# Performance work log

Hardware: AMD Instinct MI355X
Metric: run time of the kernel (lower is better)

## Reference

```python
import jax, jax.numpy as jnp
import numpy as np

MARGIN = 5.0  # margin_between_clusters


def setup_inputs() -> dict:
    key = jax.random.key(0)
    k1, k2, k3 = jax.random.split(key, 3)
    N, D, K = 262144, 128, 64
    embeddings = jax.random.normal(k1, (N, D), dtype=jnp.float32)
    cluster_labels = jax.random.randint(k2, (N,), 0, K, dtype=jnp.int64)
    centroids = jax.random.normal(k3, (K, D), dtype=jnp.float32)
    return {"embeddings": embeddings, "cluster_labels": cluster_labels, "centroids": centroids}


def reference(embeddings, cluster_labels, centroids):
    # Assumes all K clusters are present in cluster_labels (true w.h.p. for N >> K),
    # matching number_cluster = len(unique(labels)) in the original.
    N, d = embeddings.shape
    K = centroids.shape[0]
    labels = cluster_labels.astype(jnp.int32)

    x2 = jnp.sum(embeddings * embeddings, axis=1, keepdims=True)        # [N,1]
    c2 = jnp.sum(centroids * centroids, axis=1)[None, :]                # [1,K]
    d2 = jnp.maximum(x2 + c2 - 2.0 * (embeddings @ centroids.T), 0.0)  # [N,K]
    dist = jnp.sqrt(d2)

    rows = jnp.arange(N)
    own_d = dist[rows, labels]                 # distance to own centroid
    counts = jax.ops.segment_sum(jnp.ones((N,), embeddings.dtype), labels, num_segments=K)
    safe_counts = jnp.maximum(counts, 1.0)

    # attraction: per cluster, mean of squared distance to own centroid
    attr_per_cluster = jax.ops.segment_sum(own_d * own_d, labels, num_segments=K) / safe_counts
    attraction_loss = jnp.sum(jnp.where(counts > 0, attr_per_cluster, 0.0))

    # repulsion: per cluster, mean over (points_in_cluster x other_centroids) of relu((m - d)^2)
    rep = jax.nn.relu((MARGIN - dist) ** 2)    # [N,K]
    row_other = (jnp.sum(rep, axis=1) - rep[rows, labels]) / (K - 1)
    rep_per_cluster = jax.ops.segment_sum(row_other, labels, num_segments=K) / safe_counts
    repulsion_loss = jnp.sum(jnp.where(counts > 0, rep_per_cluster, 0.0))

    return (attraction_loss + repulsion_loss) / K
```

## Files before the change

kernel.cpp:

```cpp
#include <hip/hip_runtime.h>


constexpr int N = 262144;
constexpr int D = 128;
constexpr int K = 64;

constexpr int GRID = 512;
constexpr int NWAVES = 4;
constexpr int TPW = (N / 32) / (GRID * NWAVES);
constexpr int PANEL = 34 * 32;

typedef __bf16 bf16x4 __attribute__((ext_vector_type(4)));
typedef __bf16 bf16x8 __attribute__((ext_vector_type(8)));
typedef float  f32x16 __attribute__((ext_vector_type(16)));

__global__ __launch_bounds__(256) void dcl_main(
    const float* __restrict__ emb,
    const int*   __restrict__ labels,
    const float* __restrict__ cent,
    float* __restrict__ g_attr,
    float* __restrict__ g_rep,
    int*   __restrict__ g_cnt)
{
    __shared__ bf16x8 sA[2 * 8 * 64];
    __shared__ __align__(16) bf16x4 sPanel[NWAVES * PANEL];
    __shared__ float  s_c2[K];
    __shared__ float  s_attr[K];
    __shared__ float  s_rep[K];
    __shared__ int    s_cnt[K];

    const int tid  = threadIdx.x;
    const int wave = tid >> 6;
    const int lane = tid & 63;
    const int l31  = lane & 31;
    const int h    = lane >> 5;

    const int tile0 = (blockIdx.x * NWAVES + wave) * TPW;

    float4 buf[16];
    {
        const float4* src = (const float4*)emb + (size_t)tile0 * 1024 + lane;
        #pragma unroll
        for (int q = 0; q < 16; ++q) buf[q] = src[q * 64];
    }

    #pragma unroll
    for (int e = tid; e < 2 * 8 * 64; e += 256) {
        const int t = e >> 9, s = (e >> 6) & 7, l = e & 63;
        const int c  = t * 32 + (l & 31);
        const int d0 = 16 * s + 8 * (l >> 5);
        const float4 f0 = *(const float4*)(cent + c * D + d0);
        const float4 f1 = *(const float4*)(cent + c * D + d0 + 4);
        bf16x8 v;
        v[0] = (__bf16)f0.x; v[1] = (__bf16)f0.y; v[2] = (__bf16)f0.z; v[3] = (__bf16)f0.w;
        v[4] = (__bf16)f1.x; v[5] = (__bf16)f1.y; v[6] = (__bf16)f1.z; v[7] = (__bf16)f1.w;
        sA[e] = v;
    }
    if (tid < K) {
        const float4* cp = (const float4*)(cent + tid * D);
        float s = 0.f;
        #pragma unroll
        for (int q = 0; q < D / 4; ++q) {
            const float4 f = cp[q];
            s = fmaf(f.x, f.x, s); s = fmaf(f.y, f.y, s);
            s = fmaf(f.z, f.z, s); s = fmaf(f.w, f.w, s);
        }
        s_c2[tid] = s;
        s_attr[tid] = 0.f; s_rep[tid] = 0.f; s_cnt[tid] = 0;
    }
    __syncthreads();

    float c2a[16], c2b[16];
    #pragma unroll
    for (int r = 0; r < 16; ++r) {
        const int rbase = (r & 3) + 8 * (r >> 2) + 4 * h;
        c2a[r] = s_c2[rbase];
        c2b[r] = s_c2[rbase + 32];
    }

    bf16x4* panel = sPanel + wave * PANEL;

    for (int tt = 0; tt < TPW; ++tt) {
        const int tile = tile0 + tt;
        const int lbl  = labels[tile * 32 + l31];

        #pragma unroll
        for (int q = 0; q < 16; ++q) {
            bf16x4 v;
            v[0] = (__bf16)buf[q].x; v[1] = (__bf16)buf[q].y;
            v[2] = (__bf16)buf[q].z; v[3] = (__bf16)buf[q].w;
            const int n = 2 * q + h;
            panel[34 * n + l31] = v;
        }

        if (tt + 1 < TPW) {
            const float4* src = (const float4*)emb + (size_t)(tile + 1) * 1024 + lane;
            #pragma unroll
            for (int q = 0; q < 16; ++q) buf[q] = src[q * 64];
        }

        f32x16 acc0 = {0.f,0.f,0.f,0.f,0.f,0.f,0.f,0.f,0.f,0.f,0.f,0.f,0.f,0.f,0.f,0.f};
        f32x16 acc1 = {0.f,0.f,0.f,0.f,0.f,0.f,0.f,0.f,0.f,0.f,0.f,0.f,0.f,0.f,0.f,0.f};
        float x2p = 0.f;

        #pragma unroll
        for (int s = 0; s < 8; ++s) {
            const bf16x8 b = *(const bf16x8*)&panel[34 * l31 + 4 * s + 2 * h];
            #pragma unroll
            for (int e = 0; e < 8; ++e) {
                const float fe = (float)b[e];
                x2p = fmaf(fe, fe, x2p);
            }
            const bf16x8 a0 = sA[s * 64 + lane];
            const bf16x8 a1 = sA[(8 + s) * 64 + lane];
            acc0 = __builtin_amdgcn_mfma_f32_32x32x16_bf16(a0, b, acc0, 0, 0, 0);
            acc1 = __builtin_amdgcn_mfma_f32_32x32x16_bf16(a1, b, acc1, 0, 0, 0);
        }

        const float x2 = x2p + __shfl_xor(x2p, 32);

        float s1 = 0.f, s2 = 0.f, own = 0.f;
        #pragma unroll
        for (int r = 0; r < 16; ++r) {
            const int rbase = (r & 3) + 8 * (r >> 2) + 4 * h;
            {
                float d2 = fmaf(-2.f, acc0[r], x2 + c2a[r]);
                d2 = fmaxf(d2, 0.f);
                const float dd = __builtin_amdgcn_sqrtf(d2);
                s1 += dd; s2 += d2;
                if (rbase == lbl) own += d2;
            }
            {
                float d2 = fmaf(-2.f, acc1[r], x2 + c2b[r]);
                d2 = fmaxf(d2, 0.f);
                const float dd = __builtin_amdgcn_sqrtf(d2);
                s1 += dd; s2 += d2;
                if (rbase + 32 == lbl) own += d2;
            }
        }
        s1  += __shfl_xor(s1, 32);
        s2  += __shfl_xor(s2, 32);
        own += __shfl_xor(own, 32);

        if (lane < 32) {
            const float down = __builtin_amdgcn_sqrtf(own);
            const float own_term = fmaf(-10.f, down, 25.f) + own;
            const float row_other = (25.f * K - 10.f * s1 + s2 - own_term) * (1.f / (K - 1));
            atomicAdd(&s_attr[lbl], own);
            atomicAdd(&s_rep[lbl], row_other);
            atomicAdd(&s_cnt[lbl], 1);
        }
    }

    __syncthreads();
    if (tid < K) {
        atomicAdd(&g_attr[tid], s_attr[tid]);
        atomicAdd(&g_rep[tid], s_rep[tid]);
        atomicAdd(&g_cnt[tid], s_cnt[tid]);
    }
}

__global__ void dcl_finish(const float* __restrict__ g_attr,
                           const float* __restrict__ g_rep,
                           const int*   __restrict__ g_cnt,
                           float* __restrict__ out)
{
    const int k = threadIdx.x;
    const float cnt = (float)g_cnt[k];
    float v = (cnt > 0.f) ? (g_attr[k] + g_rep[k]) / cnt : 0.f;
    #pragma unroll
    for (int off = 32; off > 0; off >>= 1) v += __shfl_down(v, off);
    if (k == 0) out[0] = v * (1.f / K);
}

extern "C" void kernel_launch(void* const* d_in, const int* in_sizes, int n_in,
                              void* d_out, int out_size, void* d_ws, size_t ws_size,
                              hipStream_t stream) {
    const float* emb    = (const float*)d_in[0];
    const int*   labels = (const int*)d_in[1];
    const float* cent   = (const float*)d_in[2];
    float* out = (float*)d_out;

    float* g_attr = (float*)d_ws;
    float* g_rep  = g_attr + K;
    int*   g_cnt  = (int*)(g_rep + K);

    hipMemsetAsync(d_ws, 0, 3 * K * sizeof(float), stream);
    dcl_main<<<GRID, 256, 0, stream>>>(emb, labels, cent, g_attr, g_rep, g_cnt);
    dcl_finish<<<1, 64, 0, stream>>>(g_attr, g_rep, g_cnt, out);
}
```

Before: 205.0 us.

## Rebalance tiles over 768 blocks and seed MFMA accumulators with centroid norms

```diff
diff --git a/kernel.cpp b/kernel.cpp
--- a/kernel.cpp
+++ b/kernel.cpp
@@ -5,16 +5,17 @@
 constexpr int D = 128;
 constexpr int K = 64;
 
-constexpr int GRID = 512;
+constexpr int GRID = 768;
 constexpr int NWAVES = 4;
-constexpr int TPW = (N / 32) / (GRID * NWAVES);
+constexpr int NWTOT = GRID * NWAVES;
+constexpr int NTILES = N / 32;
 constexpr int PANEL = 34 * 32;
 
 typedef __bf16 bf16x4 __attribute__((ext_vector_type(4)));
 typedef __bf16 bf16x8 __attribute__((ext_vector_type(8)));
 typedef float  f32x16 __attribute__((ext_vector_type(16)));
 
-__global__ __launch_bounds__(256) void dcl_main(
+__global__ __launch_bounds__(256, 3) void dcl_main(
     const float* __restrict__ emb,
     const int*   __restrict__ labels,
     const float* __restrict__ cent,
@@ -25,6 +26,8 @@
     __shared__ bf16x8 sA[2 * 8 * 64];
     __shared__ __align__(16) bf16x4 sPanel[NWAVES * PANEL];
     __shared__ float  s_c2[K];
+    __shared__ __align__(16) float sC2i0[2][16];
+    __shared__ __align__(16) float sC2i1[2][16];
     __shared__ float  s_attr[K];
     __shared__ float  s_rep[K];
     __shared__ int    s_cnt[K];
@@ -35,14 +38,23 @@
     const int l31  = lane & 31;
     const int h    = lane >> 5;
 
-    const int tile0 = (blockIdx.x * NWAVES + wave) * TPW;
+    const int g = blockIdx.x * NWAVES + wave;
+    int tiles[3];
+    tiles[0] = g;
+    tiles[1] = g + NWTOT;
+    int nt = 2;
+    if (g % 3 != 2) { tiles[2] = 2 * NWTOT + (g - g / 3); nt = 3; }
 
     float4 buf[16];
     {
-        const float4* src = (const float4*)emb + (size_t)tile0 * 1024 + lane;
+        const float4* src = (const float4*)emb + (size_t)tiles[0] * 1024 + lane;
         #pragma unroll
         for (int q = 0; q < 16; ++q) buf[q] = src[q * 64];
     }
+    int lbl[3];
+    lbl[0] = labels[tiles[0] * 32 + l31];
+    lbl[1] = labels[tiles[1] * 32 + l31];
+    lbl[2] = (nt == 3) ? labels[tiles[2] * 32 + l31] : 0;
 
     #pragma unroll
     for (int e = tid; e < 2 * 8 * 64; e += 256) {
@@ -69,21 +81,17 @@
         s_attr[tid] = 0.f; s_rep[tid] = 0.f; s_cnt[tid] = 0;
     }
     __syncthreads();
-
-    float c2a[16], c2b[16];
-    #pragma unroll
-    for (int r = 0; r < 16; ++r) {
-        const int rbase = (r & 3) + 8 * (r >> 2) + 4 * h;
-        c2a[r] = s_c2[rbase];
-        c2b[r] = s_c2[rbase + 32];
-    }
+    if (tid < 32) {
+        const int hh = tid >> 4, r = tid & 15;
+        const int rb = (r & 3) + 8 * (r >> 2) + 4 * hh;
+        sC2i0[hh][r] = -0.5f * s_c2[rb];
+        sC2i1[hh][r] = -0.5f * s_c2[rb + 32];
+    }
+    __syncthreads();
 
     bf16x4* panel = sPanel + wave * PANEL;
 
-    for (int tt = 0; tt < TPW; ++tt) {
-        const int tile = tile0 + tt;
-        const int lbl  = labels[tile * 32 + l31];
-
+    for (int i = 0; i < nt; ++i) {
         #pragma unroll
         for (int q = 0; q < 16; ++q) {
             bf16x4 v;
@@ -93,14 +101,22 @@
             panel[34 * n + l31] = v;
         }
 
-        if (tt + 1 < TPW) {
-            const float4* src = (const float4*)emb + (size_t)(tile + 1) * 1024 + lane;
+        if (i + 1 < nt) {
+            const float4* src = (const float4*)emb + (size_t)tiles[i + 1] * 1024 + lane;
             #pragma unroll
             for (int q = 0; q < 16; ++q) buf[q] = src[q * 64];
         }
 
-        f32x16 acc0 = {0.f,0.f,0.f,0.f,0.f,0.f,0.f,0.f,0.f,0.f,0.f,0.f,0.f,0.f,0.f,0.f};
-        f32x16 acc1 = {0.f,0.f,0.f,0.f,0.f,0.f,0.f,0.f,0.f,0.f,0.f,0.f,0.f,0.f,0.f,0.f};
+        f32x16 acc0, acc1;
+        {
+            const float4* p0 = (const float4*)&sC2i0[h][0];
+            const float4* p1 = (const float4*)&sC2i1[h][0];
+            #pragma unroll
+            for (int w = 0; w < 4; ++w) {
+                ((float4*)&acc0)[w] = p0[w];
+                ((float4*)&acc1)[w] = p1[w];
+            }
+        }
         float x2p = 0.f;
 
         #pragma unroll
@@ -118,24 +134,25 @@
         }
 
         const float x2 = x2p + __shfl_xor(x2p, 32);
+        const int li = lbl[i];
 
         float s1 = 0.f, s2 = 0.f, own = 0.f;
         #pragma unroll
         for (int r = 0; r < 16; ++r) {
             const int rbase = (r & 3) + 8 * (r >> 2) + 4 * h;
             {
-                float d2 = fmaf(-2.f, acc0[r], x2 + c2a[r]);
+                float d2 = fmaf(-2.f, acc0[r], x2);
                 d2 = fmaxf(d2, 0.f);
                 const float dd = __builtin_amdgcn_sqrtf(d2);
                 s1 += dd; s2 += d2;
-                if (rbase == lbl) own += d2;
+                if (rbase == li) own += d2;
             }
             {
-                float d2 = fmaf(-2.f, acc1[r], x2 + c2b[r]);
+                float d2 = fmaf(-2.f, acc1[r], x2);
                 d2 = fmaxf(d2, 0.f);
                 const float dd = __builtin_amdgcn_sqrtf(d2);
                 s1 += dd; s2 += d2;
-                if (rbase + 32 == lbl) own += d2;
+                if (rbase + 32 == li) own += d2;
             }
         }
         s1  += __shfl_xor(s1, 32);
@@ -146,9 +163,9 @@
             const float down = __builtin_amdgcn_sqrtf(own);
             const float own_term = fmaf(-10.f, down, 25.f) + own;
             const float row_other = (25.f * K - 10.f * s1 + s2 - own_term) * (1.f / (K - 1));
-            atomicAdd(&s_attr[lbl], own);
-            atomicAdd(&s_rep[lbl], row_other);
-            atomicAdd(&s_cnt[lbl], 1);
+            atomicAdd(&s_attr[li], own);
+            atomicAdd(&s_rep[li], row_other);
+            atomicAdd(&s_cnt[li], 1);
         }
     }
 
```

Result: slower. 235.5 us (+14.9%).
